# Performance work log

Measured on AMD Instinct MI355X. Metric: run time of the kernel, lower is better.

The kernel has to match this reference:

```python
import jax, jax.numpy as jnp
import numpy as np

N_NODE, N_REL = 200000, 64
DIM, N_FACTOR, N_LAYER, K, B = 64, 4, 2, 32, 1024


def setup_inputs() -> dict:
    key = jax.random.key(0)
    ks = jax.random.split(key, 12)
    node_emb = jax.random.normal(ks[0], (N_NODE, N_FACTOR, DIM), jnp.float32) * 0.05
    relation_emb = jax.random.normal(ks[1], (N_REL, N_FACTOR, DIM), jnp.float32) * 0.05
    # attention MLP: Linear(2d -> d), ReLU, Linear(d -> 1); stored as [in, out]
    W1 = jax.random.normal(ks[2], (2 * DIM, DIM), jnp.float32) * (1.0 / np.sqrt(2 * DIM))
    b1 = jnp.zeros((DIM,), jnp.float32)
    W2 = jax.random.normal(ks[3], (DIM, 1), jnp.float32) * (1.0 / np.sqrt(DIM))
    b2 = jnp.zeros((1,), jnp.float32)
    users = jax.random.randint(ks[4], (B,), 0, N_NODE)
    items = jax.random.randint(ks[5], (B,), 0, N_NODE)

    def make_triple(kh, kr, kt):
        h = jax.random.randint(kh, (B, 1, N_LAYER, K), 0, N_NODE)
        r = jax.random.randint(kr, (B, 1, N_LAYER, K), 0, N_REL)
        t = jax.random.randint(kt, (B, 1, N_LAYER, K), 0, N_NODE)
        return jnp.concatenate([h, r, t], axis=1)  # [B, 3, L, K]

    users_triple = make_triple(ks[6], ks[7], ks[8])
    items_triple = make_triple(ks[9], ks[10], ks[11])
    return {
        "node_emb": node_emb, "relation_emb": relation_emb,
        "W1": W1, "b1": b1, "W2": W2, "b2": b2,
        "users": users, "items": items,
        "users_triple": users_triple, "items_triple": items_triple,
    }


def _knowledge_attention(h_emb, t_emb, W1, b1, W2, b2):
    # h_emb, t_emb: [B, L, K, F, d]
    x = jnp.concatenate([h_emb, t_emb], axis=-1)          # [B,L,K,F,2d]
    hid = jax.nn.relu(x @ W1 + b1)                        # [B,L,K,F,d]
    logits = jnp.squeeze(hid @ W2 + b2, axis=-1)          # [B,L,K,F]
    w = jax.nn.softmax(logits, axis=2)                    # softmax over neighbors K
    return jnp.sum(w[..., None] * t_emb, axis=2)          # [B,L,F,d]


def _tower(node_emb, idx, triple, W1, b1, W2, b2):
    origin = node_emb[idx]                                # [B,F,d]
    h = node_emb[triple[:, 0]]                            # [B,L,K,F,d]
    t = node_emb[triple[:, 2]]                            # [B,L,K,F,d]
    layers = _knowledge_attention(h, t, W1, b1, W2, b2)   # [B,L,F,d]
    emb = jnp.concatenate([origin[:, None], layers], axis=1)  # [B,L+1,F,d]
    return jnp.transpose(emb, (1, 0, 2, 3))               # [L+1,B,F,d]


def reference(node_emb, relation_emb, W1, b1, W2, b2, users, items, users_triple, items_triple):
    # relation_emb is gathered in the original but never used by the attention math.
    u = _tower(node_emb, users, users_triple, W1, b1, W2, b2)
    v = _tower(node_emb, items, items_triple, W1, b1, W2, b2)
    return jnp.stack([u, v])  # [2, L+1, B, F, d]
```

## Files before the change

### kernel.cpp

```cpp
#include <hip/hip_runtime.h>
#include <hip/hip_bf16.h>
#include <math.h>

#define NNODE  200000
#define DIM    64
#define NF     4
#define NLAYER 2
#define KK     32
#define BB     1024

typedef __bf16 bf16x8 __attribute__((ext_vector_type(8)));
typedef __bf16 bf16x4 __attribute__((ext_vector_type(4)));
typedef float  f32x4  __attribute__((ext_vector_type(4)));

#define XSTRIDE 136

__global__ void prep_w1t(const float* __restrict__ W1, __bf16* __restrict__ w1t) {
    int j = blockIdx.x * 256 + threadIdx.x;
    int d = j >> 7, i = j & 127;
    w1t[j] = (__bf16)W1[i * 64 + d];
}

__global__ __launch_bounds__(256, 2) void kgat_mfma(
    const float* __restrict__ node_emb,
    const __bf16* __restrict__ w1t,
    const float* __restrict__ b1,
    const float* __restrict__ W2,
    const int*   __restrict__ users,
    const int*   __restrict__ items,
    const int*   __restrict__ users_triple,
    const int*   __restrict__ items_triple,
    float*       __restrict__ out)
{
    __shared__ __bf16 Xs[128 * XSTRIDE];
    __shared__ float  logitS[128];

    const int bid   = blockIdx.x;
    const int tower = bid >> 11;
    const int b     = (bid >> 1) & 1023;
    const int layer = bid & 1;
    const int tid   = threadIdx.x;
    const int w     = tid >> 6;
    const int lane  = tid & 63;
    const int m16   = lane & 15;
    const int quad  = lane >> 4;

    const int* __restrict__ triple = tower ? items_triple : users_triple;
    const int* __restrict__ idxarr = tower ? items : users;

    const int hbase = ((b * 3 + 0) * NLAYER + layer) * KK;
    const int tbase = ((b * 3 + 2) * NLAYER + layer) * KK;

    bf16x8 Bf[4][4];
#pragma unroll
    for (int nt = 0; nt < 4; ++nt)
#pragma unroll
        for (int kt = 0; kt < 4; ++kt)
            Bf[nt][kt] = *(const bf16x8*)(w1t + (nt * 16 + m16) * 128 + kt * 32 + quad * 8);

    {
        const int m = tid & 15;
#pragma unroll
        for (int r = 0; r < 4; ++r) {
            const int task = r * 16 + (tid >> 4);
            const int k    = task & 31;
            const int ch   = task >> 5;
            const int idx  = triple[(ch ? tbase : hbase) + k];
            const float* __restrict__ src = node_emb + (size_t)idx * (NF * DIM);
#pragma unroll
            for (int j = 0; j < 4; ++j) {
                f32x4 v = *(const f32x4*)(src + j * 64 + m * 4);
                bf16x4 bv;
#pragma unroll
                for (int u = 0; u < 4; ++u) bv[u] = (__bf16)v[u];
                *(bf16x4*)(&Xs[(j * 32 + k) * XSTRIDE + ch * 64 + m * 4]) = bv;
            }
        }
    }
    __syncthreads();

    f32x4 C[2][4];
#pragma unroll
    for (int mt = 0; mt < 2; ++mt)
#pragma unroll
        for (int nt = 0; nt < 4; ++nt) C[mt][nt] = (f32x4)(0.f);

    const __bf16* Arow0 = &Xs[(w * 32 + m16) * XSTRIDE];
    const __bf16* Arow1 = &Xs[(w * 32 + 16 + m16) * XSTRIDE];
#pragma unroll
    for (int kt = 0; kt < 4; ++kt) {
        bf16x8 A0 = *(const bf16x8*)(Arow0 + kt * 32 + quad * 8);
        bf16x8 A1 = *(const bf16x8*)(Arow1 + kt * 32 + quad * 8);
#pragma unroll
        for (int nt = 0; nt < 4; ++nt) {
            C[0][nt] = __builtin_amdgcn_mfma_f32_16x16x32_bf16(A0, Bf[nt][kt], C[0][nt], 0, 0, 0);
            C[1][nt] = __builtin_amdgcn_mfma_f32_16x16x32_bf16(A1, Bf[nt][kt], C[1][nt], 0, 0, 0);
        }
    }

    float b1v[4], w2v[4];
#pragma unroll
    for (int nt = 0; nt < 4; ++nt) {
        b1v[nt] = b1[nt * 16 + m16];
        w2v[nt] = W2[nt * 16 + m16];
    }
    float lsum[2][4];
#pragma unroll
    for (int mt = 0; mt < 2; ++mt)
#pragma unroll
        for (int r = 0; r < 4; ++r) {
            float s = 0.f;
#pragma unroll
            for (int nt = 0; nt < 4; ++nt)
                s += fmaxf(C[mt][nt][r] + b1v[nt], 0.f) * w2v[nt];
            lsum[mt][r] = s;
        }
#pragma unroll
    for (int off = 1; off < 16; off <<= 1)
#pragma unroll
        for (int mt = 0; mt < 2; ++mt)
#pragma unroll
            for (int r = 0; r < 4; ++r)
                lsum[mt][r] += __shfl_xor(lsum[mt][r], off, 64);

    if (m16 == 0) {
#pragma unroll
        for (int mt = 0; mt < 2; ++mt) {
            f32x4 v;
#pragma unroll
            for (int r = 0; r < 4; ++r) v[r] = lsum[mt][r];
            *(f32x4*)&logitS[w * 32 + mt * 16 + quad * 4] = v;
        }
    }
    __syncthreads();

    const float lg = logitS[w * 32 + (lane & 31)];
    float mx = lg;
#pragma unroll
    for (int off = 16; off; off >>= 1) mx = fmaxf(mx, __shfl_xor(mx, off, 64));
    const float e = __expf(lg - mx);
    float s = e;
#pragma unroll
    for (int off = 16; off; off >>= 1) s += __shfl_xor(s, off, 64);
    const float wgt = e / s;

    float oacc = 0.f;
#pragma unroll
    for (int k = 0; k < KK; ++k) {
        const float wk = __shfl(wgt, k, 64);
        oacc += wk * (float)Xs[(w * 32 + k) * XSTRIDE + 64 + lane];
    }
    out[(((size_t)(tower * 3 + 1 + layer) * BB + b) * NF + w) * DIM + lane] = oacc;

    if (layer == 0) {
        const int oid = idxarr[b];
        out[(((size_t)(tower * 3 + 0) * BB + b) * NF + w) * DIM + lane] =
            node_emb[((size_t)oid * NF + w) * DIM + lane];
    }
}

extern "C" void kernel_launch(void* const* d_in, const int* in_sizes, int n_in,
                              void* d_out, int out_size, void* d_ws, size_t ws_size,
                              hipStream_t stream) {
    const float* node_emb     = (const float*)d_in[0];
    const float* W1           = (const float*)d_in[2];
    const float* b1           = (const float*)d_in[3];
    const float* W2           = (const float*)d_in[4];
    const float* b2           = (const float*)d_in[5]; (void)b2;
    const int*   users        = (const int*)d_in[6];
    const int*   items        = (const int*)d_in[7];
    const int*   users_triple = (const int*)d_in[8];
    const int*   items_triple = (const int*)d_in[9];
    float* out = (float*)d_out;

    __bf16* w1t = (__bf16*)d_ws;

    hipLaunchKernelGGL(prep_w1t, dim3(32), dim3(256), 0, stream, W1, w1t);
    hipLaunchKernelGGL(kgat_mfma, dim3(2 * BB * NLAYER), dim3(256), 0, stream,
                       node_emb, w1t, b1, W2,
                       users, items, users_triple, items_triple, out);
}
```

Measured before the change: 302.9 us.

## Load gathered embeddings directly into MFMA registers, dropping shared staging

Each wavefront now gathers its own factor's head/tail rows straight from global memory into MFMA A-fragment registers, and keeps the 32 tail values per lane in registers for the weighted sum, so the shared-memory X tile and both block-wide barriers are gone. W1 fragments are reloaded per k-step from global/cache rather than held across the kernel, and the launch bound rises to 3 blocks per CU. The aim is to cut LDS traffic and synchronisation and raise occupancy. The cost is that tail rows are read twice (once in bf16 for the matmul, once in fp32), register pressure is higher with the 32-entry tv array, and the logitS write and read happen within one wavefront with no barrier.

```diff
diff --git a/kernel.cpp b/kernel.cpp
--- a/kernel.cpp
+++ b/kernel.cpp
@@ -1,5 +1,4 @@
 #include <hip/hip_runtime.h>
-#include <hip/hip_bf16.h>
 #include <math.h>
 
 #define NNODE  200000
@@ -10,10 +9,7 @@
 #define BB     1024
 
 typedef __bf16 bf16x8 __attribute__((ext_vector_type(8)));
-typedef __bf16 bf16x4 __attribute__((ext_vector_type(4)));
 typedef float  f32x4  __attribute__((ext_vector_type(4)));
-
-#define XSTRIDE 136
 
 __global__ void prep_w1t(const float* __restrict__ W1, __bf16* __restrict__ w1t) {
     int j = blockIdx.x * 256 + threadIdx.x;
@@ -21,7 +17,7 @@
     w1t[j] = (__bf16)W1[i * 64 + d];
 }
 
-__global__ __launch_bounds__(256, 2) void kgat_mfma(
+__global__ __launch_bounds__(256, 3) void kgat_direct(
     const float* __restrict__ node_emb,
     const __bf16* __restrict__ w1t,
     const float* __restrict__ b1,
@@ -32,8 +28,7 @@
     const int*   __restrict__ items_triple,
     float*       __restrict__ out)
 {
-    __shared__ __bf16 Xs[128 * XSTRIDE];
-    __shared__ float  logitS[128];
+    __shared__ float logitS[128];
 
     const int bid   = blockIdx.x;
     const int tower = bid >> 11;
@@ -51,33 +46,36 @@
     const int hbase = ((b * 3 + 0) * NLAYER + layer) * KK;
     const int tbase = ((b * 3 + 2) * NLAYER + layer) * KK;
 
-    bf16x8 Bf[4][4];
+    int hi[2], ti[2];
+    hi[0] = triple[hbase + m16];
+    hi[1] = triple[hbase + 16 + m16];
+    ti[0] = triple[tbase + m16];
+    ti[1] = triple[tbase + 16 + m16];
+    const int tkv = triple[tbase + (lane & 31)];
+
+    bf16x8 Af[2][4];
 #pragma unroll
-    for (int nt = 0; nt < 4; ++nt)
+    for (int mt = 0; mt < 2; ++mt) {
+        const float* __restrict__ rh = node_emb + ((size_t)hi[mt] * NF + w) * DIM;
+        const float* __restrict__ rt = node_emb + ((size_t)ti[mt] * NF + w) * DIM;
 #pragma unroll
-        for (int kt = 0; kt < 4; ++kt)
-            Bf[nt][kt] = *(const bf16x8*)(w1t + (nt * 16 + m16) * 128 + kt * 32 + quad * 8);
-
-    {
-        const int m = tid & 15;
+        for (int kt = 0; kt < 4; ++kt) {
+            const float* __restrict__ src = (kt < 2 ? rh : rt) + (kt & 1) * 32 + quad * 8;
+            f32x4 v0 = *(const f32x4*)src;
+            f32x4 v1 = *(const f32x4*)(src + 4);
+            bf16x8 a;
 #pragma unroll
-        for (int r = 0; r < 4; ++r) {
-            const int task = r * 16 + (tid >> 4);
-            const int k    = task & 31;
-            const int ch   = task >> 5;
-            const int idx  = triple[(ch ? tbase : hbase) + k];
-            const float* __restrict__ src = node_emb + (size_t)idx * (NF * DIM);
-#pragma unroll
-            for (int j = 0; j < 4; ++j) {
-                f32x4 v = *(const f32x4*)(src + j * 64 + m * 4);
-                bf16x4 bv;
-#pragma unroll
-                for (int u = 0; u < 4; ++u) bv[u] = (__bf16)v[u];
-                *(bf16x4*)(&Xs[(j * 32 + k) * XSTRIDE + ch * 64 + m * 4]) = bv;
-            }
+            for (int u = 0; u < 4; ++u) { a[u] = (__bf16)v0[u]; a[4 + u] = (__bf16)v1[u]; }
+            Af[mt][kt] = a;
         }
     }
-    __syncthreads();
+
+    float tv[KK];
+#pragma unroll
+    for (int k = 0; k < KK; ++k) {
+        const int tk = __shfl(tkv, k, 64);
+        tv[k] = node_emb[((size_t)tk * NF + w) * DIM + lane];
+    }
 
     f32x4 C[2][4];
 #pragma unroll
@@ -85,16 +83,16 @@
 #pragma unroll
         for (int nt = 0; nt < 4; ++nt) C[mt][nt] = (f32x4)(0.f);
 
-    const __bf16* Arow0 = &Xs[(w * 32 + m16) * XSTRIDE];
-    const __bf16* Arow1 = &Xs[(w * 32 + 16 + m16) * XSTRIDE];
 #pragma unroll
     for (int kt = 0; kt < 4; ++kt) {
-        bf16x8 A0 = *(const bf16x8*)(Arow0 + kt * 32 + quad * 8);
-        bf16x8 A1 = *(const bf16x8*)(Arow1 + kt * 32 + quad * 8);
+        bf16x8 Bn[4];
+#pragma unroll
+        for (int nt = 0; nt < 4; ++nt)
+            Bn[nt] = *(const bf16x8*)(w1t + (nt * 16 + m16) * 128 + kt * 32 + quad * 8);
 #pragma unroll
         for (int nt = 0; nt < 4; ++nt) {
-            C[0][nt] = __builtin_amdgcn_mfma_f32_16x16x32_bf16(A0, Bf[nt][kt], C[0][nt], 0, 0, 0);
-            C[1][nt] = __builtin_amdgcn_mfma_f32_16x16x32_bf16(A1, Bf[nt][kt], C[1][nt], 0, 0, 0);
+            C[0][nt] = __builtin_amdgcn_mfma_f32_16x16x32_bf16(Af[0][kt], Bn[nt], C[0][nt], 0, 0, 0);
+            C[1][nt] = __builtin_amdgcn_mfma_f32_16x16x32_bf16(Af[1][kt], Bn[nt], C[1][nt], 0, 0, 0);
         }
     }
 
@@ -132,9 +130,8 @@
             *(f32x4*)&logitS[w * 32 + mt * 16 + quad * 4] = v;
         }
     }
-    __syncthreads();
+    const float lg = logitS[w * 32 + (lane & 31)];
 
-    const float lg = logitS[w * 32 + (lane & 31)];
     float mx = lg;
 #pragma unroll
     for (int off = 16; off; off >>= 1) mx = fmaxf(mx, __shfl_xor(mx, off, 64));
@@ -146,10 +143,8 @@
 
     float oacc = 0.f;
 #pragma unroll
-    for (int k = 0; k < KK; ++k) {
-        const float wk = __shfl(wgt, k, 64);
-        oacc += wk * (float)Xs[(w * 32 + k) * XSTRIDE + 64 + lane];
-    }
+    for (int k = 0; k < KK; ++k)
+        oacc += __shfl(wgt, k, 64) * tv[k];
     out[(((size_t)(tower * 3 + 1 + layer) * BB + b) * NF + w) * DIM + lane] = oacc;
 
     if (layer == 0) {
@@ -176,7 +171,7 @@
     __bf16* w1t = (__bf16*)d_ws;
 
     hipLaunchKernelGGL(prep_w1t, dim3(32), dim3(256), 0, stream, W1, w1t);
-    hipLaunchKernelGGL(kgat_mfma, dim3(2 * BB * NLAYER), dim3(256), 0, stream,
+    hipLaunchKernelGGL(kgat_direct, dim3(2 * BB * NLAYER), dim3(256), 0, stream,
                        node_emb, w1t, b1, W2,
                        users, items, users_triple, items_triple, out);
 }
```

New measurement: 322.7 us. 1.07x slower.
